# Kernel optimization log

Measured on AMD Instinct MI355X. Metric: run time of the kernel, lower is better.

## Reference

```python
import jax, jax.numpy as jnp
import numpy as np

N_NODES = 50000
N_EDGES = 800000
N_FEAT = 512
N_HID = 64
N_CLASSES = 40
N_LAYERS = 10
ALPHA = 0.8


def setup_inputs() -> dict:
    key = jax.random.key(0)
    ks = jax.random.split(key, 7)
    x = jax.random.normal(ks[0], (N_NODES, N_FEAT), dtype=jnp.float32)
    edge_index = jax.random.randint(ks[1], (2, N_EDGES), 0, N_NODES, dtype=jnp.int64)
    edge_weight = jax.random.uniform(ks[2], (N_EDGES,), dtype=jnp.float32)
    W_in = jax.random.normal(ks[3], (N_FEAT, N_HID), dtype=jnp.float32) / np.sqrt(N_FEAT)
    b_in = jnp.zeros((N_HID,), dtype=jnp.float32)
    W_out = jax.random.normal(ks[4], (N_HID, N_CLASSES), dtype=jnp.float32) / np.sqrt(N_HID)
    b_out = jnp.zeros((N_CLASSES,), dtype=jnp.float32)
    return {"x": x, "edge_index": edge_index, "edge_weight": edge_weight,
            "W_in": W_in, "b_in": b_in, "W_out": W_out, "b_out": b_out}


def _spmm(edge_index, edge_weight, h):
    # sparse adj @ h : gather source rows, scale by edge weight, scatter-add to dst
    src, dst = edge_index[0], edge_index[1]
    msgs = h[src] * edge_weight[:, None]          # [E, n_hid]
    return jax.ops.segment_sum(msgs, dst, num_segments=N_NODES)


def reference(x, edge_index, edge_weight, W_in, b_in, W_out, b_out):
    h = x @ W_in + b_in                           # linear_in: [N, n_hid]
    h0 = h
    for _ in range(N_LAYERS):
        # APPNPLayer: alpha * (adj @ h) + (1 - alpha) * h0
        h = ALPHA * _spmm(edge_index, edge_weight, h) + (1.0 - ALPHA) * h0
    return h @ W_out + b_out                      # linear_out: [N, n_classes]
```

## Files before the change

kernel.cpp:

```cpp
#include <hip/hip_runtime.h>

#define NNODES 50000
#define NEDGES 800000
#define NFEAT 512
#define NHID 64
#define NCLASSES 40
#define NLAYERS 10
#define ALPHA 0.8f

typedef unsigned int uint32;
typedef unsigned short bf16_t;
typedef __attribute__((ext_vector_type(8))) short s16x8;
typedef __attribute__((ext_vector_type(4))) float f32x4;
typedef __attribute__((ext_vector_type(4))) unsigned int u32x4;

__device__ __forceinline__ float bflo(uint32 u) { return __uint_as_float(u << 16); }
__device__ __forceinline__ float bfhi(uint32 u) { return __uint_as_float(u & 0xFFFF0000u); }
__device__ __forceinline__ bf16_t f2bf(float f) {
    uint32 u = __float_as_uint(f);
    u += 0x7FFFu + ((u >> 16) & 1u);
    return (bf16_t)(u >> 16);
}


__global__ void zero_counts_kernel(int* __restrict__ counts) {
    int i = blockIdx.x * blockDim.x + threadIdx.x;
    if (i < NNODES) counts[i] = 0;
}

__global__ void hist_kernel(const int* __restrict__ dst, int* __restrict__ counts) {
    int e = blockIdx.x * blockDim.x + threadIdx.x;
    if (e >= NEDGES) return;
    atomicAdd(&counts[dst[e]], 1);
}

__global__ void scan1_kernel(const int* __restrict__ counts,
                             int* __restrict__ row_ptr,
                             int* __restrict__ bsum) {
    __shared__ int sd[1024];
    int tid = threadIdx.x;
    int i = blockIdx.x * 1024 + tid;
    int v = (i < NNODES) ? counts[i] : 0;
    sd[tid] = v;
    __syncthreads();
    for (int off = 1; off < 1024; off <<= 1) {
        int t = (tid >= off) ? sd[tid - off] : 0;
        __syncthreads();
        sd[tid] += t;
        __syncthreads();
    }
    if (i < NNODES) row_ptr[i] = sd[tid] - v;
    if (tid == 1023) bsum[blockIdx.x] = sd[1023];
}

__global__ void scan2_kernel(const int* __restrict__ bsum, int* __restrict__ boff) {
    int tid = threadIdx.x;
    const int NB = (NNODES + 1023) / 1024;
    int v0 = (tid < NB) ? bsum[tid] : 0;
    int v = v0;
#pragma unroll
    for (int off = 1; off < 64; off <<= 1) {
        int t = __shfl_up(v, off);
        if (tid >= off) v += t;
    }
    if (tid < NB) boff[tid] = v - v0;
    if (tid == NB - 1) boff[NB] = v;
}

__global__ void scan3_kernel(const int* __restrict__ boff,
                             int* __restrict__ row_ptr,
                             int* __restrict__ cursor) {
    int i = blockIdx.x * blockDim.x + threadIdx.x;
    if (i < NNODES) {
        int rp = row_ptr[i] + boff[i >> 10];
        row_ptr[i] = rp;
        cursor[i] = rp;
    } else if (i == NNODES) {
        row_ptr[NNODES] = boff[(NNODES + 1023) / 1024];
    }
}

__global__ void csr_scatter_kernel(const int* __restrict__ src,
                                   const int* __restrict__ dst,
                                   const float* __restrict__ ew,
                                   int* __restrict__ cursor,
                                   int2* __restrict__ edata) {
    int e = blockIdx.x * blockDim.x + threadIdx.x;
    if (e >= NEDGES) return;
    int d = dst[e];
    int pos = atomicAdd(&cursor[d], 1);
    int2 ed;
    ed.x = src[e];
    ed.y = __float_as_int(ALPHA * ew[e]);
    edata[pos] = ed;
}


__global__ void prep_w_kernel(const float* __restrict__ W, bf16_t* __restrict__ wfrag) {
    int i = blockIdx.x * blockDim.x + threadIdx.x;
    if (i >= NFEAT * NHID) return;
    int k = i >> 6, n = i & 63;
    int kb = k >> 5, ko = k & 31, hi = ko >> 3, j = ko & 7;
    int nb = n >> 4, lo = n & 15;
    int lane = hi * 16 + lo;
    wfrag[(size_t)((kb * 4 + nb) * 64 + lane) * 8 + j] = f2bf(W[(size_t)k * NHID + n]);
}

__global__ __launch_bounds__(256) void linear_in_kernel(
        const float* __restrict__ x, const bf16_t* __restrict__ wfrag,
        const float* __restrict__ b, bf16_t* __restrict__ h0) {
    __shared__ u32x4 wl4[4096];
    const bf16_t* wl = (const bf16_t*)wl4;
    int tid = threadIdx.x;
    for (int i = tid; i < 4096; i += 256)
        wl4[i] = ((const u32x4*)wfrag)[i];
    __syncthreads();

    int wid = (blockIdx.x * 256 + tid) >> 6;
    if (wid >= NNODES / 16) return;
    int lane = tid & 63;
    int node0 = wid * 16;
    int row = node0 + (lane & 15);
    int khi = (lane >> 4) << 3;

    f32x4 acc[4];
#pragma unroll
    for (int nb = 0; nb < 4; ++nb) acc[nb] = (f32x4){0.f, 0.f, 0.f, 0.f};

    const float* xr = x + (size_t)row * NFEAT + khi;
#pragma unroll 4
    for (int kb = 0; kb < 16; ++kb) {
        float4 xa = *(const float4*)(xr);
        float4 xb = *(const float4*)(xr + 4);
        xr += 32;
        s16x8 a;
        a[0] = (short)f2bf(xa.x); a[1] = (short)f2bf(xa.y);
        a[2] = (short)f2bf(xa.z); a[3] = (short)f2bf(xa.w);
        a[4] = (short)f2bf(xb.x); a[5] = (short)f2bf(xb.y);
        a[6] = (short)f2bf(xb.z); a[7] = (short)f2bf(xb.w);
#pragma unroll
        for (int nb = 0; nb < 4; ++nb) {
            s16x8 bb = *(const s16x8*)(&wl[(size_t)((kb * 4 + nb) * 64 + lane) * 8]);
            acc[nb] = __builtin_amdgcn_mfma_f32_16x16x32_bf16(a, bb, acc[nb], 0, 0, 0);
        }
    }

    int chi = lane >> 4;
#pragma unroll
    for (int nb = 0; nb < 4; ++nb) {
        int col = nb * 16 + (lane & 15);
        float bias = b[col];
#pragma unroll
        for (int r = 0; r < 4; ++r) {
            int n = node0 + chi * 4 + r;
            h0[(size_t)n * NHID + col] = f2bf(acc[nb][r] + bias);
        }
    }
}


__device__ __forceinline__ void acc_edge(float* acc, u32x4 g, float wgt) {
    acc[0] = fmaf(wgt, bflo(g[0]), acc[0]);
    acc[1] = fmaf(wgt, bfhi(g[0]), acc[1]);
    acc[2] = fmaf(wgt, bflo(g[1]), acc[2]);
    acc[3] = fmaf(wgt, bfhi(g[1]), acc[3]);
    acc[4] = fmaf(wgt, bflo(g[2]), acc[4]);
    acc[5] = fmaf(wgt, bfhi(g[2]), acc[5]);
    acc[6] = fmaf(wgt, bflo(g[3]), acc[6]);
    acc[7] = fmaf(wgt, bfhi(g[3]), acc[7]);
}

__global__ __launch_bounds__(256) void spmm_pull_kernel(
        const int2* __restrict__ edata, const int* __restrict__ row_ptr,
        const bf16_t* __restrict__ h_cur, const bf16_t* __restrict__ h0,
        bf16_t* __restrict__ h_next) {
    int gid = blockIdx.x * blockDim.x + threadIdx.x;
    int wave = gid >> 6;
    int lane = threadIdx.x & 63;
    int grp = lane >> 3;
    int fl = (lane & 7) << 3;
    int node = wave * 8 + grp;
    int beg = 0, deg = 0;
    if (node < NNODES) {
        beg = row_ptr[node];
        deg = row_ptr[node + 1] - beg;
    }
    int steps = deg;
    steps = max(steps, __shfl_xor(steps, 8));
    steps = max(steps, __shfl_xor(steps, 16));
    steps = max(steps, __shfl_xor(steps, 32));

    float acc[8];
#pragma unroll
    for (int j = 0; j < 8; ++j) acc[j] = 0.f;

    int t = 0;
    for (; t + 1 < steps; t += 2) {
        bool v0 = (t < deg), v1 = (t + 1 < deg);
        int2 e0 = edata[v0 ? (beg + t) : 0];
        int2 e1 = edata[v1 ? (beg + t + 1) : 0];
        float w0 = v0 ? __int_as_float(e0.y) : 0.f;
        float w1 = v1 ? __int_as_float(e1.y) : 0.f;
        u32x4 g0 = *(const u32x4*)(h_cur + ((size_t)e0.x << 6) + fl);
        u32x4 g1 = *(const u32x4*)(h_cur + ((size_t)e1.x << 6) + fl);
        acc_edge(acc, g0, w0);
        acc_edge(acc, g1, w1);
    }
    if (t < steps) {
        bool v0 = (t < deg);
        int2 e0 = edata[v0 ? (beg + t) : 0];
        float w0 = v0 ? __int_as_float(e0.y) : 0.f;
        u32x4 g0 = *(const u32x4*)(h_cur + ((size_t)e0.x << 6) + fl);
        acc_edge(acc, g0, w0);
    }

    if (node < NNODES) {
        size_t o = ((size_t)node << 6) + fl;
        u32x4 hv = *(const u32x4*)(h0 + o);
        const float s = 1.0f - ALPHA;
        float r[8];
        r[0] = fmaf(s, bflo(hv[0]), acc[0]);
        r[1] = fmaf(s, bfhi(hv[0]), acc[1]);
        r[2] = fmaf(s, bflo(hv[1]), acc[2]);
        r[3] = fmaf(s, bfhi(hv[1]), acc[3]);
        r[4] = fmaf(s, bflo(hv[2]), acc[4]);
        r[5] = fmaf(s, bfhi(hv[2]), acc[5]);
        r[6] = fmaf(s, bflo(hv[3]), acc[6]);
        r[7] = fmaf(s, bfhi(hv[3]), acc[7]);
        u32x4 ov;
        ov[0] = (uint32)f2bf(r[0]) | ((uint32)f2bf(r[1]) << 16);
        ov[1] = (uint32)f2bf(r[2]) | ((uint32)f2bf(r[3]) << 16);
        ov[2] = (uint32)f2bf(r[4]) | ((uint32)f2bf(r[5]) << 16);
        ov[3] = (uint32)f2bf(r[6]) | ((uint32)f2bf(r[7]) << 16);
        *(u32x4*)(h_next + o) = ov;
    }
}


__global__ __launch_bounds__(256) void linear_out_kernel(
        const bf16_t* __restrict__ h, const float* __restrict__ W,
        const float* __restrict__ b, float* __restrict__ out) {
    __shared__ float wsh[NHID * NCLASSES];
    __shared__ float bs[NCLASSES];
    int tid = threadIdx.x;
    for (int i = tid; i < NHID * NCLASSES; i += 256) wsh[i] = W[i];
    if (tid < NCLASSES) bs[tid] = b[tid];
    __syncthreads();
    int node = blockIdx.x * 256 + tid;
    if (node >= NNODES) return;
    float acc[NCLASSES];
#pragma unroll
    for (int c = 0; c < NCLASSES; ++c) acc[c] = bs[c];
    const bf16_t* hr = h + (size_t)node * NHID;
#pragma unroll
    for (int q = 0; q < 8; ++q) {
        u32x4 v = *(const u32x4*)(hr + q * 8);
        float hv[8];
        hv[0] = bflo(v[0]); hv[1] = bfhi(v[0]);
        hv[2] = bflo(v[1]); hv[3] = bfhi(v[1]);
        hv[4] = bflo(v[2]); hv[5] = bfhi(v[2]);
        hv[6] = bflo(v[3]); hv[7] = bfhi(v[3]);
#pragma unroll
        for (int kk = 0; kk < 8; ++kk) {
#pragma unroll
            for (int c = 0; c < NCLASSES; ++c)
                acc[c] = fmaf(hv[kk], wsh[(q * 8 + kk) * NCLASSES + c], acc[c]);
        }
    }
    float* op = out + (size_t)node * NCLASSES;
#pragma unroll
    for (int c = 0; c < NCLASSES; c += 4)
        *(float4*)(op + c) = make_float4(acc[c], acc[c + 1], acc[c + 2], acc[c + 3]);
}

extern "C" void kernel_launch(void* const* d_in, const int* in_sizes, int n_in,
                              void* d_out, int out_size, void* d_ws, size_t ws_size,
                              hipStream_t stream) {
    const float* x     = (const float*)d_in[0];
    const int*   ei    = (const int*)d_in[1];
    const float* ew    = (const float*)d_in[2];
    const float* W_in  = (const float*)d_in[3];
    const float* b_in  = (const float*)d_in[4];
    const float* W_out = (const float*)d_in[5];
    const float* b_out = (const float*)d_in[6];
    float* out = (float*)d_out;

    const int HN = NNODES * NHID;
    bf16_t* h0 = (bf16_t*)d_ws;
    bf16_t* ha = h0 + HN;
    bf16_t* hb = ha + HN;
    bf16_t* wfrag = hb + HN;
    int2* edata   = (int2*)(wfrag + NFEAT * NHID);
    int*  row_ptr = (int*)(edata + NEDGES);
    int*  cursor  = row_ptr + (NNODES + 1);
    int*  counts  = cursor + NNODES;
    int*  bsum    = counts + NNODES;
    int*  boff    = bsum + 64;

    const int* src = ei;
    const int* dst = ei + NEDGES;

    zero_counts_kernel<<<(NNODES + 255) / 256, 256, 0, stream>>>(counts);
    hist_kernel<<<(NEDGES + 255) / 256, 256, 0, stream>>>(dst, counts);
    const int NB = (NNODES + 1023) / 1024;
    scan1_kernel<<<NB, 1024, 0, stream>>>(counts, row_ptr, bsum);
    scan2_kernel<<<1, 64, 0, stream>>>(bsum, boff);
    scan3_kernel<<<(NNODES + 256) / 256, 256, 0, stream>>>(boff, row_ptr, cursor);
    csr_scatter_kernel<<<(NEDGES + 255) / 256, 256, 0, stream>>>(src, dst, ew, cursor, edata);

    prep_w_kernel<<<(NFEAT * NHID + 255) / 256, 256, 0, stream>>>(W_in, wfrag);
    const int GEMM_BLOCKS = (NNODES / 16 + 3) / 4;
    linear_in_kernel<<<GEMM_BLOCKS, 256, 0, stream>>>(x, wfrag, b_in, h0);

    const int NWAVES = (NNODES + 7) / 8;
    const int SPMM_BLOCKS = (NWAVES * 64 + 255) / 256;
    bf16_t* cur = h0;
    bf16_t* nxt = ha;
    for (int l = 0; l < NLAYERS; ++l) {
        spmm_pull_kernel<<<SPMM_BLOCKS, 256, 0, stream>>>(edata, row_ptr, cur, h0, nxt);
        cur = nxt;
        nxt = (cur == ha) ? hb : ha;
    }

    linear_out_kernel<<<(NNODES + 255) / 256, 256, 0, stream>>>(cur, W_out, b_out, out);
}
```

Baseline: 320.0 us.

## Split SpMM into two source-half passes and pack edge data to 32 bits

Edges in the CSR are partitioned by whether the source node is in the first or second half of the nodes. Each APPNP layer then runs two pull passes, so each pass gathers from only half of the hidden feature matrix, which is meant to fit better in L2. Edge records are compressed to 32 bits: a 16-bit source index plus a bf16 weight. Loads and stores are also marked nontemporal. In exchange, there are twice as many kernel launches, an extra read and write of the intermediate output per layer, and extra bf16 rounding of the weights and partial sums.

```diff
diff --git a/kernel.cpp b/kernel.cpp
--- a/kernel.cpp
+++ b/kernel.cpp
@@ -7,6 +7,7 @@
 #define NCLASSES 40
 #define NLAYERS 10
 #define ALPHA 0.8f
+#define HALF 25000
 
 typedef unsigned int uint32;
 typedef unsigned short bf16_t;
@@ -25,22 +26,24 @@
 
 __global__ void zero_counts_kernel(int* __restrict__ counts) {
     int i = blockIdx.x * blockDim.x + threadIdx.x;
-    if (i < NNODES) counts[i] = 0;
-}
-
-__global__ void hist_kernel(const int* __restrict__ dst, int* __restrict__ counts) {
+    if (i < 2 * NNODES) counts[i] = 0;
+}
+
+__global__ void hist_kernel(const int* __restrict__ src, const int* __restrict__ dst,
+                            int* __restrict__ countsA, int* __restrict__ countsB) {
     int e = blockIdx.x * blockDim.x + threadIdx.x;
     if (e >= NEDGES) return;
-    atomicAdd(&counts[dst[e]], 1);
-}
-
-__global__ void scan1_kernel(const int* __restrict__ counts,
-                             int* __restrict__ row_ptr,
-                             int* __restrict__ bsum) {
+    int d = dst[e];
+    if (src[e] < HALF) atomicAdd(&countsA[d], 1);
+    else               atomicAdd(&countsB[d], 1);
+}
+
+__global__ void scan1_kernel(const int* __restrict__ countsA, const int* __restrict__ countsB,
+                             int* __restrict__ row_ptr, int* __restrict__ bsum) {
     __shared__ int sd[1024];
     int tid = threadIdx.x;
     int i = blockIdx.x * 1024 + tid;
-    int v = (i < NNODES) ? counts[i] : 0;
+    int v = (i < NNODES) ? (countsA[i] + countsB[i]) : 0;
     sd[tid] = v;
     __syncthreads();
     for (int off = 1; off < 1024; off <<= 1) {
@@ -67,32 +70,32 @@
     if (tid == NB - 1) boff[NB] = v;
 }
 
-__global__ void scan3_kernel(const int* __restrict__ boff,
-                             int* __restrict__ row_ptr,
-                             int* __restrict__ cursor) {
+__global__ void scan3_kernel(const int* __restrict__ boff, const int* __restrict__ countsA,
+                             int* __restrict__ row_ptr, int* __restrict__ split,
+                             int* __restrict__ cursorA, int* __restrict__ cursorB) {
     int i = blockIdx.x * blockDim.x + threadIdx.x;
     if (i < NNODES) {
         int rp = row_ptr[i] + boff[i >> 10];
+        int sp = rp + countsA[i];
         row_ptr[i] = rp;
-        cursor[i] = rp;
+        split[i] = sp;
+        cursorA[i] = rp;
+        cursorB[i] = sp;
     } else if (i == NNODES) {
         row_ptr[NNODES] = boff[(NNODES + 1023) / 1024];
     }
 }
 
-__global__ void csr_scatter_kernel(const int* __restrict__ src,
-                                   const int* __restrict__ dst,
+__global__ void csr_scatter_kernel(const int* __restrict__ src, const int* __restrict__ dst,
                                    const float* __restrict__ ew,
-                                   int* __restrict__ cursor,
-                                   int2* __restrict__ edata) {
+                                   int* __restrict__ cursorA, int* __restrict__ cursorB,
+                                   uint32* __restrict__ edata) {
     int e = blockIdx.x * blockDim.x + threadIdx.x;
     if (e >= NEDGES) return;
     int d = dst[e];
-    int pos = atomicAdd(&cursor[d], 1);
-    int2 ed;
-    ed.x = src[e];
-    ed.y = __float_as_int(ALPHA * ew[e]);
-    edata[pos] = ed;
+    int s = src[e];
+    int pos = (s < HALF) ? atomicAdd(&cursorA[d], 1) : atomicAdd(&cursorB[d], 1);
+    edata[pos] = (uint32)s | ((uint32)f2bf(ALPHA * ew[e]) << 16);
 }
 
 
@@ -170,8 +173,10 @@
     acc[7] = fmaf(wgt, bfhi(g[3]), acc[7]);
 }
 
-__global__ __launch_bounds__(256) void spmm_pull_kernel(
-        const int2* __restrict__ edata, const int* __restrict__ row_ptr,
+template <int FIRST>
+__global__ __launch_bounds__(256) void spmm_pass_kernel(
+        const uint32* __restrict__ edata, const int* __restrict__ row_ptr,
+        const int* __restrict__ split,
         const bf16_t* __restrict__ h_cur, const bf16_t* __restrict__ h0,
         bf16_t* __restrict__ h_next) {
     int gid = blockIdx.x * blockDim.x + threadIdx.x;
@@ -182,8 +187,9 @@
     int node = wave * 8 + grp;
     int beg = 0, deg = 0;
     if (node < NNODES) {
-        beg = row_ptr[node];
-        deg = row_ptr[node + 1] - beg;
+        beg = FIRST ? row_ptr[node] : split[node];
+        int end = FIRST ? split[node] : row_ptr[node + 1];
+        deg = end - beg;
     }
     int steps = deg;
     steps = max(steps, __shfl_xor(steps, 8));
@@ -197,42 +203,54 @@
     int t = 0;
     for (; t + 1 < steps; t += 2) {
         bool v0 = (t < deg), v1 = (t + 1 < deg);
-        int2 e0 = edata[v0 ? (beg + t) : 0];
-        int2 e1 = edata[v1 ? (beg + t + 1) : 0];
-        float w0 = v0 ? __int_as_float(e0.y) : 0.f;
-        float w1 = v1 ? __int_as_float(e1.y) : 0.f;
-        u32x4 g0 = *(const u32x4*)(h_cur + ((size_t)e0.x << 6) + fl);
-        u32x4 g1 = *(const u32x4*)(h_cur + ((size_t)e1.x << 6) + fl);
+        uint32 e0 = __builtin_nontemporal_load(edata + (v0 ? (beg + t) : 0));
+        uint32 e1 = __builtin_nontemporal_load(edata + (v1 ? (beg + t + 1) : 0));
+        float w0 = v0 ? bfhi(e0) : 0.f;
+        float w1 = v1 ? bfhi(e1) : 0.f;
+        u32x4 g0 = *(const u32x4*)(h_cur + ((size_t)(e0 & 0xFFFFu) << 6) + fl);
+        u32x4 g1 = *(const u32x4*)(h_cur + ((size_t)(e1 & 0xFFFFu) << 6) + fl);
         acc_edge(acc, g0, w0);
         acc_edge(acc, g1, w1);
     }
     if (t < steps) {
         bool v0 = (t < deg);
-        int2 e0 = edata[v0 ? (beg + t) : 0];
-        float w0 = v0 ? __int_as_float(e0.y) : 0.f;
-        u32x4 g0 = *(const u32x4*)(h_cur + ((size_t)e0.x << 6) + fl);
+        uint32 e0 = __builtin_nontemporal_load(edata + (v0 ? (beg + t) : 0));
+        float w0 = v0 ? bfhi(e0) : 0.f;
+        u32x4 g0 = *(const u32x4*)(h_cur + ((size_t)(e0 & 0xFFFFu) << 6) + fl);
         acc_edge(acc, g0, w0);
     }
 
     if (node < NNODES) {
         size_t o = ((size_t)node << 6) + fl;
-        u32x4 hv = *(const u32x4*)(h0 + o);
-        const float s = 1.0f - ALPHA;
         float r[8];
-        r[0] = fmaf(s, bflo(hv[0]), acc[0]);
-        r[1] = fmaf(s, bfhi(hv[0]), acc[1]);
-        r[2] = fmaf(s, bflo(hv[1]), acc[2]);
-        r[3] = fmaf(s, bfhi(hv[1]), acc[3]);
-        r[4] = fmaf(s, bflo(hv[2]), acc[4]);
-        r[5] = fmaf(s, bfhi(hv[2]), acc[5]);
-        r[6] = fmaf(s, bflo(hv[3]), acc[6]);
-        r[7] = fmaf(s, bfhi(hv[3]), acc[7]);
+        if (FIRST) {
+            u32x4 hv = __builtin_nontemporal_load((const u32x4*)(h0 + o));
+            const float s = 1.0f - ALPHA;
+            r[0] = fmaf(s, bflo(hv[0]), acc[0]);
+            r[1] = fmaf(s, bfhi(hv[0]), acc[1]);
+            r[2] = fmaf(s, bflo(hv[1]), acc[2]);
+            r[3] = fmaf(s, bfhi(hv[1]), acc[3]);
+            r[4] = fmaf(s, bflo(hv[2]), acc[4]);
+            r[5] = fmaf(s, bfhi(hv[2]), acc[5]);
+            r[6] = fmaf(s, bflo(hv[3]), acc[6]);
+            r[7] = fmaf(s, bfhi(hv[3]), acc[7]);
+        } else {
+            u32x4 hv = __builtin_nontemporal_load((const u32x4*)(h_next + o));
+            r[0] = bflo(hv[0]) + acc[0];
+            r[1] = bfhi(hv[0]) + acc[1];
+            r[2] = bflo(hv[1]) + acc[2];
+            r[3] = bfhi(hv[1]) + acc[3];
+            r[4] = bflo(hv[2]) + acc[4];
+            r[5] = bfhi(hv[2]) + acc[5];
+            r[6] = bflo(hv[3]) + acc[6];
+            r[7] = bfhi(hv[3]) + acc[7];
+        }
         u32x4 ov;
         ov[0] = (uint32)f2bf(r[0]) | ((uint32)f2bf(r[1]) << 16);
         ov[1] = (uint32)f2bf(r[2]) | ((uint32)f2bf(r[3]) << 16);
         ov[2] = (uint32)f2bf(r[4]) | ((uint32)f2bf(r[5]) << 16);
         ov[3] = (uint32)f2bf(r[6]) | ((uint32)f2bf(r[7]) << 16);
-        *(u32x4*)(h_next + o) = ov;
+        __builtin_nontemporal_store(ov, (u32x4*)(h_next + o));
     }
 }
 
@@ -290,23 +308,29 @@
     bf16_t* ha = h0 + HN;
     bf16_t* hb = ha + HN;
     bf16_t* wfrag = hb + HN;
-    int2* edata   = (int2*)(wfrag + NFEAT * NHID);
-    int*  row_ptr = (int*)(edata + NEDGES);
-    int*  cursor  = row_ptr + (NNODES + 1);
-    int*  counts  = cursor + NNODES;
-    int*  bsum    = counts + NNODES;
-    int*  boff    = bsum + 64;
+    uint32* edata  = (uint32*)(wfrag + NFEAT * NHID);
+    int* row_ptr = (int*)(edata + NEDGES);
+    int* split   = row_ptr + (NNODES + 1);
+    int* cursorA = split + NNODES;
+    int* cursorB = cursorA + NNODES;
+    int* counts  = cursorB + NNODES;
+    int* bsum    = counts + 2 * NNODES;
+    int* boff    = bsum + 64;
 
     const int* src = ei;
     const int* dst = ei + NEDGES;
-
-    zero_counts_kernel<<<(NNODES + 255) / 256, 256, 0, stream>>>(counts);
-    hist_kernel<<<(NEDGES + 255) / 256, 256, 0, stream>>>(dst, counts);
+    int* countsA = counts;
+    int* countsB = counts + NNODES;
+
+    zero_counts_kernel<<<(2 * NNODES + 255) / 256, 256, 0, stream>>>(counts);
+    hist_kernel<<<(NEDGES + 255) / 256, 256, 0, stream>>>(src, dst, countsA, countsB);
     const int NB = (NNODES + 1023) / 1024;
-    scan1_kernel<<<NB, 1024, 0, stream>>>(counts, row_ptr, bsum);
+    scan1_kernel<<<NB, 1024, 0, stream>>>(countsA, countsB, row_ptr, bsum);
     scan2_kernel<<<1, 64, 0, stream>>>(bsum, boff);
-    scan3_kernel<<<(NNODES + 256) / 256, 256, 0, stream>>>(boff, row_ptr, cursor);
-    csr_scatter_kernel<<<(NEDGES + 255) / 256, 256, 0, stream>>>(src, dst, ew, cursor, edata);
+    scan3_kernel<<<(NNODES + 256) / 256, 256, 0, stream>>>(
+        boff, countsA, row_ptr, split, cursorA, cursorB);
+    csr_scatter_kernel<<<(NEDGES + 255) / 256, 256, 0, stream>>>(
+        src, dst, ew, cursorA, cursorB, edata);
 
     prep_w_kernel<<<(NFEAT * NHID + 255) / 256, 256, 0, stream>>>(W_in, wfrag);
     const int GEMM_BLOCKS = (NNODES / 16 + 3) / 4;
@@ -317,7 +341,10 @@
     bf16_t* cur = h0;
     bf16_t* nxt = ha;
     for (int l = 0; l < NLAYERS; ++l) {
-        spmm_pull_kernel<<<SPMM_BLOCKS, 256, 0, stream>>>(edata, row_ptr, cur, h0, nxt);
+        spmm_pass_kernel<1><<<SPMM_BLOCKS, 256, 0, stream>>>(
+            edata, row_ptr, split, cur, h0, nxt);
+        spmm_pass_kernel<0><<<SPMM_BLOCKS, 256, 0, stream>>>(
+            edata, row_ptr, split, cur, h0, nxt);
         cur = nxt;
         nxt = (cur == ha) ? hb : ha;
     }
```

Result: slower. 438.1 us (+36.9%).

## Pack CSR edge records into 32 bits and unroll SpMM gather by four

Applied to the files above, without the earlier changes.

Each CSR edge record shrinks from an int2 (source index plus fp32 weight) to one 32-bit word: a 16-bit source index and a bf16 weight scaled by alpha. This halves the edge-array traffic on every propagation layer. The pull SpMM loop is also unrolled from two to four edges per step, so more independent row gathers are in flight. The trade-off is reduced precision in edge weights, and the index packing only holds while the node count fits in 16 bits (50000 here).

```diff
diff --git a/kernel.cpp b/kernel.cpp
--- a/kernel.cpp
+++ b/kernel.cpp
@@ -84,15 +84,12 @@
                                    const int* __restrict__ dst,
                                    const float* __restrict__ ew,
                                    int* __restrict__ cursor,
-                                   int2* __restrict__ edata) {
+                                   uint32* __restrict__ edata) {
     int e = blockIdx.x * blockDim.x + threadIdx.x;
     if (e >= NEDGES) return;
     int d = dst[e];
     int pos = atomicAdd(&cursor[d], 1);
-    int2 ed;
-    ed.x = src[e];
-    ed.y = __float_as_int(ALPHA * ew[e]);
-    edata[pos] = ed;
+    edata[pos] = (uint32)src[e] | ((uint32)f2bf(ALPHA * ew[e]) << 16);
 }
 
 
@@ -171,7 +168,7 @@
 }
 
 __global__ __launch_bounds__(256) void spmm_pull_kernel(
-        const int2* __restrict__ edata, const int* __restrict__ row_ptr,
+        const uint32* __restrict__ edata, const int* __restrict__ row_ptr,
         const bf16_t* __restrict__ h_cur, const bf16_t* __restrict__ h0,
         bf16_t* __restrict__ h_next) {
     int gid = blockIdx.x * blockDim.x + threadIdx.x;
@@ -195,22 +192,30 @@
     for (int j = 0; j < 8; ++j) acc[j] = 0.f;
 
     int t = 0;
-    for (; t + 1 < steps; t += 2) {
-        bool v0 = (t < deg), v1 = (t + 1 < deg);
-        int2 e0 = edata[v0 ? (beg + t) : 0];
-        int2 e1 = edata[v1 ? (beg + t + 1) : 0];
-        float w0 = v0 ? __int_as_float(e0.y) : 0.f;
-        float w1 = v1 ? __int_as_float(e1.y) : 0.f;
-        u32x4 g0 = *(const u32x4*)(h_cur + ((size_t)e0.x << 6) + fl);
-        u32x4 g1 = *(const u32x4*)(h_cur + ((size_t)e1.x << 6) + fl);
+    for (; t + 3 < steps; t += 4) {
+        bool v0 = (t < deg), v1 = (t + 1 < deg), v2 = (t + 2 < deg), v3 = (t + 3 < deg);
+        uint32 e0 = edata[v0 ? (beg + t) : 0];
+        uint32 e1 = edata[v1 ? (beg + t + 1) : 0];
+        uint32 e2 = edata[v2 ? (beg + t + 2) : 0];
+        uint32 e3 = edata[v3 ? (beg + t + 3) : 0];
+        float w0 = v0 ? bfhi(e0) : 0.f;
+        float w1 = v1 ? bfhi(e1) : 0.f;
+        float w2 = v2 ? bfhi(e2) : 0.f;
+        float w3 = v3 ? bfhi(e3) : 0.f;
+        u32x4 g0 = *(const u32x4*)(h_cur + ((size_t)(e0 & 0xFFFFu) << 6) + fl);
+        u32x4 g1 = *(const u32x4*)(h_cur + ((size_t)(e1 & 0xFFFFu) << 6) + fl);
+        u32x4 g2 = *(const u32x4*)(h_cur + ((size_t)(e2 & 0xFFFFu) << 6) + fl);
+        u32x4 g3 = *(const u32x4*)(h_cur + ((size_t)(e3 & 0xFFFFu) << 6) + fl);
         acc_edge(acc, g0, w0);
         acc_edge(acc, g1, w1);
-    }
-    if (t < steps) {
+        acc_edge(acc, g2, w2);
+        acc_edge(acc, g3, w3);
+    }
+    for (; t < steps; ++t) {
         bool v0 = (t < deg);
-        int2 e0 = edata[v0 ? (beg + t) : 0];
-        float w0 = v0 ? __int_as_float(e0.y) : 0.f;
-        u32x4 g0 = *(const u32x4*)(h_cur + ((size_t)e0.x << 6) + fl);
+        uint32 e0 = edata[v0 ? (beg + t) : 0];
+        float w0 = v0 ? bfhi(e0) : 0.f;
+        u32x4 g0 = *(const u32x4*)(h_cur + ((size_t)(e0 & 0xFFFFu) << 6) + fl);
         acc_edge(acc, g0, w0);
     }
 
@@ -290,12 +295,12 @@
     bf16_t* ha = h0 + HN;
     bf16_t* hb = ha + HN;
     bf16_t* wfrag = hb + HN;
-    int2* edata   = (int2*)(wfrag + NFEAT * NHID);
-    int*  row_ptr = (int*)(edata + NEDGES);
-    int*  cursor  = row_ptr + (NNODES + 1);
-    int*  counts  = cursor + NNODES;
-    int*  bsum    = counts + NNODES;
-    int*  boff    = bsum + 64;
+    uint32* edata  = (uint32*)(wfrag + NFEAT * NHID);
+    int* row_ptr = (int*)(edata + NEDGES);
+    int* cursor  = row_ptr + (NNODES + 1);
+    int* counts  = cursor + NNODES;
+    int* bsum    = counts + NNODES;
+    int* boff    = bsum + 64;
 
     const int* src = ei;
     const int* dst = ei + NEDGES;
```

Measured after the change: 304.1 us. -5.0%, faster.
